# Performance work log

Measured on AMD Instinct MI355X. Metric: run time of the kernel, lower is better.

## Reference

```python
import jax, jax.numpy as jnp
import numpy as np

H, N, L, BATCH = 128, 64, 4096, 8


def _make_dplr_hippo(n):
    # HiPPO-LegS -> NPLR -> DPLR diagonalization (float64 numpy, as in torch source)
    ar = np.arange(n, dtype=np.float64)
    p0 = np.sqrt(1.0 + 2.0 * ar)
    A = p0[:, None] * p0[None, :]
    A = np.tril(A) - np.diag(ar)
    nhippo = -A
    Pv = np.sqrt(ar + 0.5)
    Bv = np.sqrt(2.0 * ar + 1.0)
    S = nhippo + Pv[:, None] * Pv[None, :]
    Lambda_real = np.mean(np.diag(S)) * np.ones(n)
    Lambda_imag, V = np.linalg.eigh(S * -1j)
    V = V.astype(np.complex64)
    P = (V.conj().T @ Pv.astype(np.complex64))
    B = (V.conj().T @ Bv.astype(np.complex64))
    Lam = (Lambda_real + 1j * Lambda_imag).astype(np.complex64)
    return Lam, P, B


def _ri(x):  # complex -> [..., 2] real view (like torch.view_as_real)
    return np.stack([x.real, x.imag], axis=-1).astype(np.float32)


def setup_inputs() -> dict:
    key = jax.random.key(0)
    k_u, k_c, k_d = jax.random.split(key, 3)
    Lam, P, B = _make_dplr_hippo(N)
    Lambda_ri = np.tile(_ri(Lam)[None], (H, 1, 1))          # [H, N, 2]
    P_ri = np.tile(_ri(P)[None], (H, 1, 1))                 # [H, N, 2]
    B_ri = np.tile(_ri(B)[None], (H, 1, 1))                 # [H, N, 2]
    C_ri = jax.random.normal(k_c, (H, N, 2), dtype=jnp.float32)
    D = jax.random.normal(k_d, (H, 1), dtype=jnp.float32)
    u = jax.random.normal(k_u, (BATCH, L, H), dtype=jnp.float32)
    step = jnp.array([1.0 / L], dtype=jnp.float32)
    return {
        "u": u,
        "B_ri": jnp.asarray(B_ri),
        "C_ri": jnp.asarray(C_ri),
        "D": D,
        "Lambda_ri": jnp.asarray(Lambda_ri),
        "P_ri": jnp.asarray(P_ri),
        "step": step,
    }


def _as_c(x_ri):
    return jax.lax.complex(x_ri[..., 0], x_ri[..., 1])


def reference(u, B_ri, C_ri, D, Lambda_ri, P_ri, step):
    Bc = _as_c(B_ri)        # [H, N] complex64
    Cc = _as_c(C_ri)        # [H, N]
    Lam = _as_c(Lambda_ri)  # [H, N]
    Pc = _as_c(P_ri)        # [H, N]
    batch, seq_len, h = u.shape

    # roots of unity and bilinear-transform terms
    z = jnp.exp(-2j * jnp.pi * jnp.arange(seq_len) / seq_len)   # [L] complex64
    g = (2.0 / step).astype(jnp.complex64) * ((1.0 - z) / (1.0 + z))  # [L]
    c = 2.0 / (1.0 + z)                                          # [L]

    # Cauchy resolvent, shared by the four cauchy_dot reductions: [H, L, N]
    r = 1.0 / (g[None, :, None] - Lam[:, None, :])

    def cauchy(v):  # v: [H, N] -> [H, L]
        return jnp.einsum("hn,hln->hl", v, r)

    k00 = cauchy(jnp.conj(Cc) * Bc)
    k01 = cauchy(jnp.conj(Cc) * Pc)
    k10 = cauchy(jnp.conj(Pc) * Bc)
    k11 = cauchy(jnp.conj(Pc) * Pc)
    at_roots = c[None, :] * (k00 - k01 * (1.0 / (1.0 + k11)) * k10)  # [H, L]

    kernel = jnp.fft.ifft(at_roots, n=seq_len, axis=-1).real  # [H, L] float32

    # linear (full) FFT convolution, length 2L-1, keep first L samples
    nfft = 2 * seq_len - 1
    u_f = jnp.fft.rfft(u, n=nfft, axis=1)                 # [B, F, H]
    k_f = jnp.fft.rfft(kernel, n=nfft, axis=-1)           # [H, F]
    y = jnp.fft.irfft(u_f * k_f.T[None], n=nfft, axis=1)[:, :seq_len, :]  # [B, L, H]

    return y + u @ D  # D: [H,1] -> broadcast add of skip term
```

## Files before the change

kernel.cpp:

```cpp
#include <hip/hip_runtime.h>
#include <hip/hip_bf16.h>
#include <hip/hip_fp16.h>
#include <math.h>

#define HH 128
#define NN 64
#define LL 4096
#define BB 8
#define NFFT 8192
#define KSTR 4160

#define CAU_BLOCKS 1024
#define TRU_BLOCKS 4096
#define SKP_BLOCKS 8192

__device__ __forceinline__ float2 cmul(float2 a, float2 b) {
    return make_float2(a.x * b.x - a.y * b.y, a.x * b.y + a.y * b.x);
}
__device__ __forceinline__ float2 cadd(float2 a, float2 b) {
    return make_float2(a.x + b.x, a.y + b.y);
}
__device__ __forceinline__ float2 csub(float2 a, float2 b) {
    return make_float2(a.x - b.x, a.y - b.y);
}
__device__ __forceinline__ int brev13(int x) { return (int)(__brev((unsigned)x) >> 19); }
__device__ __forceinline__ int brev10(int x) { return (int)(__brev((unsigned)x) >> 22); }
__device__ __forceinline__ int swz(int v) { return v ^ ((v >> 4) & 15); }

__device__ __forceinline__ int k_of_slot(int s) {
    if (s >= 4096) return 3584;
    int t = s >> 3, j = s & 7;
    if (t == 0) {
        const int tab[8] = {0, 1024, 2048, 3072, 4096, 512, 1536, 2560};
        return tab[j];
    }
    return (j < 4) ? j * 1024 + t : (j - 4) * 1024 + 1024 - t;
}

__device__ __forceinline__ float2 twid(float rev, float sg) {
    return make_float2(__builtin_amdgcn_cosf(rev), sg * __builtin_amdgcn_sinf(rev));
}


__device__ __forceinline__ void bfly8_dif(float2 x[8], float jf, float inv2m,
                                          float inv4m, float inv8m, float sg) {
    const float s2 = 0.70710678118654752f;
    float2 w8 = twid(jf * inv8m, sg);
    float2 w4 = twid(jf * inv4m, sg);
    float2 w2 = twid(jf * inv2m, sg);
    float2 e1 = make_float2(s2, sg * s2);
    float2 e3 = make_float2(-s2, sg * s2);
    float2 y0 = cadd(x[0], x[4]), y1 = cadd(x[1], x[5]);
    float2 y2 = cadd(x[2], x[6]), y3 = cadd(x[3], x[7]);
    float2 t0 = csub(x[0], x[4]), t1 = csub(x[1], x[5]);
    float2 t2 = csub(x[2], x[6]), t3 = csub(x[3], x[7]);
    float2 w8i = make_float2(-sg * w8.y, sg * w8.x);
    float2 z0 = cmul(w8, t0);
    float2 z1 = cmul(cmul(w8, e1), t1);
    float2 z2 = cmul(w8i, t2);
    float2 z3 = cmul(cmul(w8, e3), t3);
    {
        float2 a0 = cadd(y0, y2);
        float2 a2 = cmul(w4, csub(y0, y2));
        float2 a1 = cadd(y1, y3);
        float2 t = cmul(w4, csub(y1, y3));
        float2 a3 = make_float2(-sg * t.y, sg * t.x);
        x[0] = cadd(a0, a1);
        x[1] = cmul(w2, csub(a0, a1));
        x[2] = cadd(a2, a3);
        x[3] = cmul(w2, csub(a2, a3));
    }
    {
        float2 a0 = cadd(z0, z2);
        float2 a2 = cmul(w4, csub(z0, z2));
        float2 a1 = cadd(z1, z3);
        float2 t = cmul(w4, csub(z1, z3));
        float2 a3 = make_float2(-sg * t.y, sg * t.x);
        x[4] = cadd(a0, a1);
        x[5] = cmul(w2, csub(a0, a1));
        x[6] = cadd(a2, a3);
        x[7] = cmul(w2, csub(a2, a3));
    }
}

__device__ __forceinline__ void bfly8_dit(float2 x[8], float jf, float inv2m,
                                          float inv4m, float inv8m, float sg) {
    const float s2 = 0.70710678118654752f;
    float2 wA = twid(jf * inv2m, sg);
    float2 wB = twid(jf * inv4m, sg);
    float2 wC = twid(jf * inv8m, sg);
    float2 t;
    t = cmul(wA, x[1]); float2 b0 = cadd(x[0], t), b1 = csub(x[0], t);
    t = cmul(wA, x[3]); float2 b2 = cadd(x[2], t), b3 = csub(x[2], t);
    t = cmul(wA, x[5]); float2 b4 = cadd(x[4], t), b5 = csub(x[4], t);
    t = cmul(wA, x[7]); float2 b6 = cadd(x[6], t), b7 = csub(x[6], t);
    float2 wBi = make_float2(-sg * wB.y, sg * wB.x);
    t = cmul(wB, b2);  float2 c0 = cadd(b0, t), c2 = csub(b0, t);
    t = cmul(wBi, b3); float2 c1 = cadd(b1, t), c3 = csub(b1, t);
    t = cmul(wB, b6);  float2 c4 = cadd(b4, t), c6 = csub(b4, t);
    t = cmul(wBi, b7); float2 c5 = cadd(b5, t), c7 = csub(b5, t);
    float2 e1 = make_float2(s2, sg * s2);
    float2 e3 = make_float2(-s2, sg * s2);
    float2 w1 = cmul(wC, e1);
    float2 w2_ = make_float2(-sg * wC.y, sg * wC.x);
    float2 w3 = cmul(wC, e3);
    t = cmul(wC, c4);  x[0] = cadd(c0, t); x[4] = csub(c0, t);
    t = cmul(w1, c5);  x[1] = cadd(c1, t); x[5] = csub(c1, t);
    t = cmul(w2_, c6); x[2] = cadd(c2, t); x[6] = csub(c2, t);
    t = cmul(w3, c7);  x[3] = cadd(c3, t); x[7] = csub(c3, t);
}

__device__ __forceinline__ void pairpt(float2& P, float2& Q, float2 K0, float2 K1) {
    float2 U0 = make_float2(0.5f * (P.x + Q.x), 0.5f * (P.y - Q.y));
    float2 U1 = make_float2(0.5f * (P.y + Q.y), 0.5f * (Q.x - P.x));
    float2 A = cmul(U0, K0);
    float2 C = cmul(U1, K1);
    P = make_float2(A.x - C.y, A.y + C.x);
    Q = make_float2(A.x + C.y, C.x - A.y);
}
__device__ __forceinline__ void selfpt(float2& P, float2 K0, float2 K1) {
    float2 U0 = make_float2(P.x, 0.f);
    float2 U1 = make_float2(P.y, 0.f);
    float2 A = cmul(U0, K0);
    float2 C = cmul(U1, K1);
    P = make_float2(A.x - C.y, A.y + C.x);
}


template <int M>
__device__ __forceinline__ void dif_f8(float2* d, int N, int tid, int nt, float sg) {
    const float inv2m = 1.0f / (2.0f * (float)M);
    const float inv4m = 1.0f / (4.0f * (float)M);
    const float inv8m = 1.0f / (8.0f * (float)M);
    for (int q = tid; q < (N >> 3); q += nt) {
        int j = q & (M - 1);
        int i0 = ((q & ~(M - 1)) << 3) + j;
        float2 x[8];
#pragma unroll
        for (int k = 0; k < 8; ++k) x[k] = d[swz(i0 + k * M)];
        bfly8_dif(x, (float)j, inv2m, inv4m, inv8m, sg);
#pragma unroll
        for (int k = 0; k < 8; ++k) d[swz(i0 + k * M)] = x[k];
    }
    __syncthreads();
}

template <int M>
__device__ __forceinline__ void dit_f8(float2* d, int N, int tid, int nt, float sg) {
    const float inv2m = 1.0f / (2.0f * (float)M);
    const float inv4m = 1.0f / (4.0f * (float)M);
    const float inv8m = 1.0f / (8.0f * (float)M);
    for (int q = tid; q < (N >> 3); q += nt) {
        int j = q & (M - 1);
        int i0 = ((q & ~(M - 1)) << 3) + j;
        float2 x[8];
#pragma unroll
        for (int k = 0; k < 8; ++k) x[k] = d[swz(i0 + k * M)];
        bfly8_dit(x, (float)j, inv2m, inv4m, inv8m, sg);
#pragma unroll
        for (int k = 0; k < 8; ++k) d[swz(i0 + k * M)] = x[k];
    }
    __syncthreads();
}

__global__ __launch_bounds__(256, 8) void stage1_kernel(
    const float* __restrict__ u,
    const float* __restrict__ B_ri, const float* __restrict__ C_ri,
    const float* __restrict__ D,
    const float* __restrict__ Lambda_ri, const float* __restrict__ P_ri,
    const float* __restrict__ step,
    float2* __restrict__ at_g, float2* __restrict__ ut2, float* __restrict__ skip) {
    __shared__ float4 smem4[264];
    const int bid = blockIdx.x;
    const int tid = threadIdx.x;

    if (bid < CAU_BLOCKS) {
        float* v11f = (float*)(smem4 + 128);
        const int h = bid >> 3;
        if (tid < NN) {
            int n = tid;
            float2 C = ((const float2*)C_ri)[h * NN + n];
            float2 Bv = ((const float2*)B_ri)[h * NN + n];
            float2 P = ((const float2*)P_ri)[h * NN + n];
            float2 lam = ((const float2*)Lambda_ri)[h * NN + n];
            float2 Cc = make_float2(C.x, -C.y);
            float2 Pc = make_float2(P.x, -P.y);
            float2 v00 = cmul(Cc, Bv);
            float2 v01 = cmul(Cc, P);
            float2 v10 = cmul(Pc, Bv);
            smem4[2 * n + 0] = make_float4(lam.x, lam.y, v00.x, v00.y);
            smem4[2 * n + 1] = make_float4(v01.x, v01.y, v10.x, v10.y);
            v11f[n] = P.x * P.x + P.y * P.y;
        }
        __syncthreads();

        const int lbase = ((bid & 7) << 8) | tid;
        const float two_over_step = 2.0f / step[0];
        float gr[2], gi[2], ccx[2], ccy[2];
#pragma unroll
        for (int p = 0; p < 2; ++p) {
            int l = lbase + p * 2048;
            double th = -6.283185307179586476925286766559 * (double)l / (double)LL;
            float sn, cs;
            sincosf((float)th, &sn, &cs);
            float dr = 1.0f + cs, di = sn;
            float inv = __builtin_amdgcn_rcpf(dr * dr + di * di);
            float nr = 1.0f - cs, ni = -sn;
            gr[p] = two_over_step * (nr * dr + ni * di) * inv;
            gi[p] = two_over_step * (ni * dr - nr * di) * inv;
            ccx[p] = 2.0f * dr * inv;
            ccy[p] = -2.0f * di * inv;
        }

        float2 k00[2], k01[2], k10[2], k11[2];
#pragma unroll
        for (int p = 0; p < 2; ++p) {
            k00[p] = make_float2(0.f, 0.f);
            k01[p] = make_float2(0.f, 0.f);
            k10[p] = make_float2(0.f, 0.f);
            k11[p] = make_float2(0.f, 0.f);
        }
#pragma unroll 4
        for (int n = 0; n < NN; ++n) {
            float4 tA = smem4[2 * n + 0];
            float4 tB = smem4[2 * n + 1];
            float w11 = v11f[n];
#pragma unroll
            for (int p = 0; p < 2; ++p) {
                float ar = gr[p] - tA.x, ai = gi[p] - tA.y;
                float id = __builtin_amdgcn_rcpf(ar * ar + ai * ai);
                float2 r = make_float2(ar * id, -ai * id);
                k00[p] = cadd(k00[p], cmul(make_float2(tA.z, tA.w), r));
                k01[p] = cadd(k01[p], cmul(make_float2(tB.x, tB.y), r));
                k10[p] = cadd(k10[p], cmul(make_float2(tB.z, tB.w), r));
                k11[p].x += w11 * r.x;
                k11[p].y += w11 * r.y;
            }
        }
#pragma unroll
        for (int p = 0; p < 2; ++p) {
            float wr = 1.0f + k11[p].x, wi = k11[p].y;
            float iw = __builtin_amdgcn_rcpf(wr * wr + wi * wi);
            float2 winv = make_float2(wr * iw, -wi * iw);
            float2 t = cmul(cmul(k01[p], winv), k10[p]);
            float2 at = cmul(make_float2(ccx[p], ccy[p]),
                             make_float2(k00[p].x - t.x, k00[p].y - t.y));
            at_g[(size_t)h * LL + lbase + p * 2048] = at;
        }
    } else if (bid < CAU_BLOCKS + TRU_BLOCKS) {
        float* tile = (float*)smem4;
        int tb = bid - CAU_BLOCKS;
        int b = tb >> 9;
        int hq = (tb >> 7) & 3;
        int h0 = hq * 32;
        int l0 = (tb & 127) * 32;
        int tx = tid & 31, ty = tid >> 5;
        const float* up = u + (size_t)b * LL * HH;
        for (int i = ty; i < 32; i += 8)
            tile[i * 33 + tx] = up[(size_t)(l0 + i) * HH + h0 + tx];
        __syncthreads();
        float2* utp = ut2 + (size_t)b * 64 * LL;
#pragma unroll
        for (int i = ty; i < 16; i += 8) {
            int c = (h0 >> 1) + i;
            float2 v = make_float2(tile[tx * 33 + 2 * i], tile[tx * 33 + 2 * i + 1]);
            utp[(size_t)c * LL + l0 + tx] = v;
        }
    } else {
        int sb = bid - (CAU_BLOCKS + TRU_BLOCKS);
        int wid = tid >> 6, lane = tid & 63;
        int row = sb * 4 + wid;
        const float* ur = u + (size_t)row * HH;
        float v = ur[lane] * D[lane] + ur[lane + 64] * D[lane + 64];
        for (int off = 32; off > 0; off >>= 1) v += __shfl_down(v, off, 64);
        if (lane == 0) skip[row] = v;
    }
}

__global__ __launch_bounds__(1024) void kfreq_kernel(const float2* __restrict__ at_g,
                                                     float2* __restrict__ KfP) {
    __shared__ float2 sm[NFFT];
    const int h = blockIdx.x;
    const int tid = threadIdx.x;
    const float2* ap = at_g + (size_t)h * LL;
#pragma unroll
    for (int it = 0; it < 4; ++it) {
        int t = tid + it * 1024;
        int l = ((t & 63) << 6) | (t >> 6);
        sm[swz((int)(__brev((unsigned)l) >> 20))] = ap[l];
    }
    __syncthreads();

    dit_f8<1>(sm, 4096, tid, 1024, +1.f);
    dit_f8<8>(sm, 4096, tid, 1024, +1.f);
    dit_f8<64>(sm, 4096, tid, 1024, +1.f);
    dit_f8<512>(sm, 4096, tid, 1024, +1.f);

    const float inv8192 = 1.0f / 8192.0f;
    for (int t = tid; t < 4096; t += 1024) {
        float kv = sm[swz(t)].x * (1.0f / 4096.0f);
        float2 w = twid((float)t * inv8192, -1.f);
        sm[swz(t)] = make_float2(kv, 0.f);
        sm[swz(t + 4096)] = make_float2(kv * w.x, kv * w.y);
    }
    __syncthreads();

    dif_f8<512>(sm, 8192, tid, 1024, -1.f);
    dif_f8<64>(sm, 8192, tid, 1024, -1.f);
    dif_f8<8>(sm, 8192, tid, 1024, -1.f);
    dif_f8<1>(sm, 8192, tid, 1024, -1.f);

    float2* kfp = KfP + (size_t)h * KSTR;
    for (int s = tid; s <= 4096; s += 1024)
        kfp[s] = sm[swz(brev13(k_of_slot(s)))];
}

__global__ __launch_bounds__(512) void conv_fft_kernel(const float2* __restrict__ ut2,
                                                       const float2* __restrict__ KfP,
                                                       __half2* __restrict__ yt2) {
    __shared__ float2 sm[NFFT];
    const int b = blockIdx.x >> 6;
    const int c = blockIdx.x & 63;
    const int h0 = 2 * c, h1 = 2 * c + 1;
    const int tid = threadIdx.x;
    const float2* up2 = ut2 + ((size_t)b * 64 + c) * LL;
    const float inv8192 = 1.0f / 8192.0f;

    for (int i = tid; i < 4096; i += 512) {
        float2 a = up2[i];
        float2 w = twid((float)i * inv8192, -1.f);
        sm[swz(i)] = a;
        sm[swz(i + 4096)] = cmul(w, a);
    }
    __syncthreads();

    dif_f8<512>(sm, 8192, tid, 512, -1.f);
    dif_f8<64>(sm, 8192, tid, 512, -1.f);
    dif_f8<8>(sm, 8192, tid, 512, -1.f);

    {
        const int m = tid;
        const int qa = (m == 0) ? 0 : brev10(m);
        const int qb = (m == 0) ? 1 : brev10(1024 - m);
        float2 xa[8], xb[8];
#pragma unroll
        for (int j = 0; j < 8; ++j) {
            xa[j] = sm[swz(8 * qa + j)];
            xb[j] = sm[swz(8 * qb + j)];
        }
        bfly8_dif(xa, 0.f, 0.5f, 0.25f, 0.125f, -1.f);
        bfly8_dif(xb, 0.f, 0.5f, 0.25f, 0.125f, -1.f);

        const float2* kf0 = KfP + (size_t)h0 * KSTR;
        const float2* kf1 = KfP + (size_t)h1 * KSTR;
        float2 K0[8], K1[8];
        {
            const float4* a4 = (const float4*)(kf0 + 8 * m);
            const float4* b4 = (const float4*)(kf1 + 8 * m);
#pragma unroll
            for (int s = 0; s < 4; ++s) {
                float4 v0 = a4[s], v1 = b4[s];
                K0[2 * s] = make_float2(v0.x, v0.y);
                K0[2 * s + 1] = make_float2(v0.z, v0.w);
                K1[2 * s] = make_float2(v1.x, v1.y);
                K1[2 * s + 1] = make_float2(v1.z, v1.w);
            }
        }
        if (m == 0) {
            selfpt(xa[0], K0[0], K1[0]);
            pairpt(xa[4], xa[7], K0[1], K1[1]);
            pairpt(xa[2], xa[3], K0[2], K1[2]);
            pairpt(xa[6], xa[5], K0[3], K1[3]);
            selfpt(xa[1], K0[4], K1[4]);
            pairpt(xb[0], xb[7], K0[5], K1[5]);
            pairpt(xb[4], xb[3], K0[6], K1[6]);
            pairpt(xb[2], xb[5], K0[7], K1[7]);
            pairpt(xb[6], xb[1], kf0[4096], kf1[4096]);
        } else {
            pairpt(xa[0], xb[7], K0[0], K1[0]);
            pairpt(xa[4], xb[3], K0[1], K1[1]);
            pairpt(xa[2], xb[5], K0[2], K1[2]);
            pairpt(xa[6], xb[1], K0[3], K1[3]);
            pairpt(xb[0], xa[7], K0[4], K1[4]);
            pairpt(xb[4], xa[3], K0[5], K1[5]);
            pairpt(xb[2], xa[5], K0[6], K1[6]);
            pairpt(xb[6], xa[1], K0[7], K1[7]);
        }
        bfly8_dit(xa, 0.f, 0.5f, 0.25f, 0.125f, +1.f);
        bfly8_dit(xb, 0.f, 0.5f, 0.25f, 0.125f, +1.f);
#pragma unroll
        for (int j = 0; j < 8; ++j) {
            sm[swz(8 * qa + j)] = xa[j];
            sm[swz(8 * qb + j)] = xb[j];
        }
    }
    __syncthreads();

    dit_f8<8>(sm, 8192, tid, 512, +1.f);
    dit_f8<64>(sm, 8192, tid, 512, +1.f);
    dit_f8<512>(sm, 8192, tid, 512, +1.f);

    __half2* yp = yt2 + ((size_t)b * 64 + c) * LL;
    const float invN = 1.0f / (float)NFFT;
    for (int x = tid; x < 4096; x += 512) {
        float2 w = twid((float)x * inv8192, +1.f);
        float2 a = sm[swz(x)];
        float2 bb = cmul(w, sm[swz(x + 4096)]);
        yp[x] = __floats2half2_rn((a.x + bb.x) * invN, (a.y + bb.y) * invN);
    }
}

__global__ __launch_bounds__(256) void transpose_y_kernel(const __half2* __restrict__ yt2,
                                                          const float* __restrict__ skip,
                                                          float* __restrict__ y) {
    __shared__ __half2 tile[32 * 17];
    int b = blockIdx.z;
    int c0 = blockIdx.x * 16;
    int l0 = blockIdx.y * 32;
    int tx = threadIdx.x, ty = threadIdx.y;
    const __half2* ytp = yt2 + (size_t)b * 64 * LL;
    const float* skp = skip + (size_t)b * LL;
    float* yp = y + (size_t)b * LL * HH;
    for (int i = ty; i < 16; i += 8)
        tile[tx * 17 + i] = ytp[(size_t)(c0 + i) * LL + l0 + tx];
    __syncthreads();
    int h0 = c0 * 2;
    for (int i = ty; i < 32; i += 8) {
        int l = l0 + i;
        float sk = skp[l];
        float2 f = __half22float2(tile[i * 17 + (tx >> 1)]);
        float v = (tx & 1) ? f.y : f.x;
        yp[(size_t)l * HH + h0 + tx] = v + sk;
    }
}

extern "C" void kernel_launch(void* const* d_in, const int* in_sizes, int n_in,
                              void* d_out, int out_size, void* d_ws, size_t ws_size,
                              hipStream_t stream) {
    const float* u = (const float*)d_in[0];
    const float* B_ri = (const float*)d_in[1];
    const float* C_ri = (const float*)d_in[2];
    const float* D = (const float*)d_in[3];
    const float* Lambda_ri = (const float*)d_in[4];
    const float* P_ri = (const float*)d_in[5];
    const float* step = (const float*)d_in[6];
    float* out = (float*)d_out;

    char* ws = (char*)d_ws;
    float2* KfP = (float2*)ws;
    float* skip = (float*)(ws + (size_t)6 * 1024 * 1024);
    float2* ut2 = (float2*)(ws + (size_t)8 * 1024 * 1024);
    char* hi = ws + (size_t)24 * 1024 * 1024;
    float2* at_g = (float2*)hi;
    __half2* yt2 = (__half2*)hi;

    stage1_kernel<<<dim3(CAU_BLOCKS + TRU_BLOCKS + SKP_BLOCKS), dim3(256), 0, stream>>>(
        u, B_ri, C_ri, D, Lambda_ri, P_ri, step, at_g, ut2, skip);
    kfreq_kernel<<<dim3(HH), dim3(1024), 0, stream>>>(at_g, KfP);
    conv_fft_kernel<<<dim3(BB * HH / 2), dim3(512), 0, stream>>>(ut2, KfP, yt2);
    transpose_y_kernel<<<dim3(HH / 32, LL / 32, BB), dim3(32, 8), 0, stream>>>(yt2, skip, out);
}
```

Before: 90.84 us.

## Switch conv FFT to radix-16 passes and simplify spectral pointwise product

The convolution kernel's 8192-point FFT changes from four radix-8 passes each way, with a fused final pass plus pointwise product, to three radix-16 passes each way. The spectral multiply becomes a separate strided loop over conjugate pairs, and the kernel-spectrum output ordering is changed to match. The goal is fewer shared-memory round trips and barriers. The cost is 16 live complex values per thread, which raises register pressure, and launch_bounds now asks for 4 blocks per CU.

```diff
diff --git a/kernel.cpp b/kernel.cpp
--- a/kernel.cpp
+++ b/kernel.cpp
@@ -24,18 +24,10 @@
     return make_float2(a.x - b.x, a.y - b.y);
 }
 __device__ __forceinline__ int brev13(int x) { return (int)(__brev((unsigned)x) >> 19); }
-__device__ __forceinline__ int brev10(int x) { return (int)(__brev((unsigned)x) >> 22); }
+__device__ __forceinline__ int kkmap(int t) {
+    return (t < 4096) ? (((t & 63) << 6) | (t >> 6)) : 4096;
+}
 __device__ __forceinline__ int swz(int v) { return v ^ ((v >> 4) & 15); }
-
-__device__ __forceinline__ int k_of_slot(int s) {
-    if (s >= 4096) return 3584;
-    int t = s >> 3, j = s & 7;
-    if (t == 0) {
-        const int tab[8] = {0, 1024, 2048, 3072, 4096, 512, 1536, 2560};
-        return tab[j];
-    }
-    return (j < 4) ? j * 1024 + t : (j - 4) * 1024 + 1024 - t;
-}
 
 __device__ __forceinline__ float2 twid(float rev, float sg) {
     return make_float2(__builtin_amdgcn_cosf(rev), sg * __builtin_amdgcn_sinf(rev));
@@ -110,20 +102,85 @@
     t = cmul(w3, c7);  x[3] = cadd(c3, t); x[7] = csub(c3, t);
 }
 
-__device__ __forceinline__ void pairpt(float2& P, float2& Q, float2 K0, float2 K1) {
-    float2 U0 = make_float2(0.5f * (P.x + Q.x), 0.5f * (P.y - Q.y));
-    float2 U1 = make_float2(0.5f * (P.y + Q.y), 0.5f * (Q.x - P.x));
-    float2 A = cmul(U0, K0);
-    float2 C = cmul(U1, K1);
-    P = make_float2(A.x - C.y, A.y + C.x);
-    Q = make_float2(A.x + C.y, C.x - A.y);
-}
-__device__ __forceinline__ void selfpt(float2& P, float2 K0, float2 K1) {
-    float2 U0 = make_float2(P.x, 0.f);
-    float2 U1 = make_float2(P.y, 0.f);
-    float2 A = cmul(U0, K0);
-    float2 C = cmul(U1, K1);
-    P = make_float2(A.x - C.y, A.y + C.x);
+
+__device__ __forceinline__ void make_wk16(float2 wk[8], float2 w16, float sg) {
+    const float c1 = 0.92387953251128675613f;
+    const float s1 = 0.38268343236508977173f;
+    const float s2 = 0.70710678118654752440f;
+    wk[0] = w16;
+    wk[1] = cmul(w16, make_float2(c1, sg * s1));
+    wk[2] = cmul(w16, make_float2(s2, sg * s2));
+    wk[3] = cmul(w16, make_float2(s1, sg * c1));
+    wk[4] = make_float2(-sg * w16.y, sg * w16.x);
+    wk[5] = cmul(w16, make_float2(-s1, sg * c1));
+    wk[6] = cmul(w16, make_float2(-s2, sg * s2));
+    wk[7] = cmul(w16, make_float2(-c1, sg * s1));
+}
+
+__device__ __forceinline__ void bfly16_dif(float2 x[16], float jf, float invm, float sg) {
+    const float inv2m = 0.5f * invm, inv4m = 0.25f * invm;
+    const float inv8m = 0.125f * invm, inv16m = 0.0625f * invm;
+    float2 wk[8];
+    make_wk16(wk, twid(jf * inv16m, sg), sg);
+    float2 y[8], z[8];
+#pragma unroll
+    for (int k = 0; k < 8; ++k) {
+        y[k] = cadd(x[k], x[k + 8]);
+        z[k] = cmul(wk[k], csub(x[k], x[k + 8]));
+    }
+    bfly8_dif(y, jf, inv2m, inv4m, inv8m, sg);
+    bfly8_dif(z, jf, inv2m, inv4m, inv8m, sg);
+#pragma unroll
+    for (int k = 0; k < 8; ++k) { x[k] = y[k]; x[k + 8] = z[k]; }
+}
+
+__device__ __forceinline__ void bfly16_dit(float2 x[16], float jf, float invm, float sg) {
+    const float inv2m = 0.5f * invm, inv4m = 0.25f * invm;
+    const float inv8m = 0.125f * invm, inv16m = 0.0625f * invm;
+    bfly8_dit(x, jf, inv2m, inv4m, inv8m, sg);
+    bfly8_dit(x + 8, jf, inv2m, inv4m, inv8m, sg);
+    float2 wk[8];
+    make_wk16(wk, twid(jf * inv16m, sg), sg);
+#pragma unroll
+    for (int k = 0; k < 8; ++k) {
+        float2 t = cmul(wk[k], x[k + 8]);
+        float2 lo = x[k];
+        x[k] = cadd(lo, t);
+        x[k + 8] = csub(lo, t);
+    }
+}
+
+
+template <int M>
+__device__ __forceinline__ void dif_f16(float2* d, int N, int tid, int nt, float sg) {
+    const float invm = 1.0f / (float)M;
+    for (int q = tid; q < (N >> 4); q += nt) {
+        int j = q & (M - 1);
+        int i0 = ((q & ~(M - 1)) << 4) + j;
+        float2 x[16];
+#pragma unroll
+        for (int k = 0; k < 16; ++k) x[k] = d[swz(i0 + k * M)];
+        bfly16_dif(x, (float)j, invm, sg);
+#pragma unroll
+        for (int k = 0; k < 16; ++k) d[swz(i0 + k * M)] = x[k];
+    }
+    __syncthreads();
+}
+
+template <int M>
+__device__ __forceinline__ void dit_f16(float2* d, int N, int tid, int nt, float sg) {
+    const float invm = 1.0f / (float)M;
+    for (int q = tid; q < (N >> 4); q += nt) {
+        int j = q & (M - 1);
+        int i0 = ((q & ~(M - 1)) << 4) + j;
+        float2 x[16];
+#pragma unroll
+        for (int k = 0; k < 16; ++k) x[k] = d[swz(i0 + k * M)];
+        bfly16_dit(x, (float)j, invm, sg);
+#pragma unroll
+        for (int k = 0; k < 16; ++k) d[swz(i0 + k * M)] = x[k];
+    }
+    __syncthreads();
 }
 
 
@@ -311,13 +368,12 @@
     dif_f8<1>(sm, 8192, tid, 1024, -1.f);
 
     float2* kfp = KfP + (size_t)h * KSTR;
-    for (int s = tid; s <= 4096; s += 1024)
-        kfp[s] = sm[swz(brev13(k_of_slot(s)))];
-}
-
-__global__ __launch_bounds__(512) void conv_fft_kernel(const float2* __restrict__ ut2,
-                                                       const float2* __restrict__ KfP,
-                                                       __half2* __restrict__ yt2) {
+    for (int t = tid; t <= 4096; t += 1024) kfp[t] = sm[swz(brev13(kkmap(t)))];
+}
+
+__global__ __launch_bounds__(512, 4) void conv_fft_kernel(const float2* __restrict__ ut2,
+                                                          const float2* __restrict__ KfP,
+                                                          __half2* __restrict__ yt2) {
     __shared__ float2 sm[NFFT];
     const int b = blockIdx.x >> 6;
     const int c = blockIdx.x & 63;
@@ -334,71 +390,33 @@
     }
     __syncthreads();
 
-    dif_f8<512>(sm, 8192, tid, 512, -1.f);
-    dif_f8<64>(sm, 8192, tid, 512, -1.f);
-    dif_f8<8>(sm, 8192, tid, 512, -1.f);
-
-    {
-        const int m = tid;
-        const int qa = (m == 0) ? 0 : brev10(m);
-        const int qb = (m == 0) ? 1 : brev10(1024 - m);
-        float2 xa[8], xb[8];
-#pragma unroll
-        for (int j = 0; j < 8; ++j) {
-            xa[j] = sm[swz(8 * qa + j)];
-            xb[j] = sm[swz(8 * qb + j)];
-        }
-        bfly8_dif(xa, 0.f, 0.5f, 0.25f, 0.125f, -1.f);
-        bfly8_dif(xb, 0.f, 0.5f, 0.25f, 0.125f, -1.f);
-
-        const float2* kf0 = KfP + (size_t)h0 * KSTR;
-        const float2* kf1 = KfP + (size_t)h1 * KSTR;
-        float2 K0[8], K1[8];
-        {
-            const float4* a4 = (const float4*)(kf0 + 8 * m);
-            const float4* b4 = (const float4*)(kf1 + 8 * m);
-#pragma unroll
-            for (int s = 0; s < 4; ++s) {
-                float4 v0 = a4[s], v1 = b4[s];
-                K0[2 * s] = make_float2(v0.x, v0.y);
-                K0[2 * s + 1] = make_float2(v0.z, v0.w);
-                K1[2 * s] = make_float2(v1.x, v1.y);
-                K1[2 * s + 1] = make_float2(v1.z, v1.w);
-            }
-        }
-        if (m == 0) {
-            selfpt(xa[0], K0[0], K1[0]);
-            pairpt(xa[4], xa[7], K0[1], K1[1]);
-            pairpt(xa[2], xa[3], K0[2], K1[2]);
-            pairpt(xa[6], xa[5], K0[3], K1[3]);
-            selfpt(xa[1], K0[4], K1[4]);
-            pairpt(xb[0], xb[7], K0[5], K1[5]);
-            pairpt(xb[4], xb[3], K0[6], K1[6]);
-            pairpt(xb[2], xb[5], K0[7], K1[7]);
-            pairpt(xb[6], xb[1], kf0[4096], kf1[4096]);
-        } else {
-            pairpt(xa[0], xb[7], K0[0], K1[0]);
-            pairpt(xa[4], xb[3], K0[1], K1[1]);
-            pairpt(xa[2], xb[5], K0[2], K1[2]);
-            pairpt(xa[6], xb[1], K0[3], K1[3]);
-            pairpt(xb[0], xa[7], K0[4], K1[4]);
-            pairpt(xb[4], xa[3], K0[5], K1[5]);
-            pairpt(xb[2], xa[5], K0[6], K1[6]);
-            pairpt(xb[6], xa[1], K0[7], K1[7]);
-        }
-        bfly8_dit(xa, 0.f, 0.5f, 0.25f, 0.125f, +1.f);
-        bfly8_dit(xb, 0.f, 0.5f, 0.25f, 0.125f, +1.f);
-#pragma unroll
-        for (int j = 0; j < 8; ++j) {
-            sm[swz(8 * qa + j)] = xa[j];
-            sm[swz(8 * qb + j)] = xb[j];
-        }
-    }
-    __syncthreads();
-
-    dit_f8<8>(sm, 8192, tid, 512, +1.f);
-    dit_f8<64>(sm, 8192, tid, 512, +1.f);
-    dit_f8<512>(sm, 8192, tid, 512, +1.f);
+    dif_f16<256>(sm, 8192, tid, 512, -1.f);
+    dif_f16<16>(sm, 8192, tid, 512, -1.f);
+    dif_f16<1>(sm, 8192, tid, 512, -1.f);
+
+    const float2* kf0 = KfP + (size_t)h0 * KSTR;
+    const float2* kf1 = KfP + (size_t)h1 * KSTR;
+    for (int t = tid; t <= 4096; t += 512) {
+        int kk = kkmap(t);
+        bool self = (kk == 0) || (kk == 4096);
+        int p = swz(brev13(kk));
+        int q = self ? p : swz(brev13(NFFT - kk));
+        float2 K0 = kf0[t];
+        float2 K1 = kf1[t];
+        float2 Zp = sm[p];
+        float2 Zq = sm[q];
+        float2 U0 = make_float2(0.5f * (Zp.x + Zq.x), 0.5f * (Zp.y - Zq.y));
+        float2 U1 = make_float2(0.5f * (Zp.y + Zq.y), 0.5f * (Zq.x - Zp.x));
+        float2 A = cmul(U0, K0);
+        float2 C = cmul(U1, K1);
+        sm[p] = make_float2(A.x - C.y, A.y + C.x);
+        if (!self) sm[q] = make_float2(A.x + C.y, C.x - A.y);
+    }
+    __syncthreads();
+
+    dit_f16<1>(sm, 8192, tid, 512, +1.f);
+    dit_f16<16>(sm, 8192, tid, 512, +1.f);
+    dit_f16<256>(sm, 8192, tid, 512, +1.f);
 
     __half2* yp = yt2 + ((size_t)b * 64 + c) * LL;
     const float invN = 1.0f / (float)NFFT;
```

New measurement: 79.76 us. 1.14x faster.
